# Optimization experiments

Hardware: AMD Instinct MI355X
Metric: run time of the kernel (lower is better)

The kernel has to match this reference:

```python
import jax, jax.numpy as jnp
import numpy as np

LOG_GAIN = 2.5
CLIP_LIMIT = 1.0
GRID = (8, 8)
NBINS = 256
KS = 5
SIGMA_COLOR = 0.1
SIGMA_SPACE = 1.0
SIGMA_G = 1.0


def _gauss1d(ks, sigma):
    x = jnp.arange(ks, dtype=jnp.float32) - ks // 2
    g = jnp.exp(-(x * x) / (2.0 * sigma * sigma))
    return g / g.sum()


def normalize01(x):
    mn, mx = x.min(), x.max()
    return (x - mn) / (mx - mn)


def adjust_log(x, gain):
    # kornia.enhance.adjust_log with clip_output=True
    return jnp.clip(gain * jnp.log2(1.0 + x), 0.0, 1.0)


def equalize_clahe(x, clip_limit, grid, nbins):
    B, C, H, W = x.shape
    GH, GW = grid
    th, tw = H // GH, W // GW
    pixels = th * tw
    # per-tile histograms via flat scatter-add (T = B*C*GH*GW tiles)
    tiles = x.reshape(B, C, GH, th, GW, tw).transpose(0, 1, 2, 4, 3, 5).reshape(-1, pixels)
    bins_t = jnp.clip((tiles * nbins).astype(jnp.int32), 0, nbins - 1)
    T = bins_t.shape[0]
    flat = (jnp.arange(T, dtype=jnp.int32)[:, None] * nbins + bins_t).ravel()
    hist = jnp.zeros((T * nbins,), jnp.float32).at[flat].add(1.0).reshape(T, nbins)
    # clip histogram and redistribute excess uniformly (kornia/OpenCV style)
    max_val = max(int(clip_limit * pixels // nbins), 1)
    clipped = jnp.minimum(hist, float(max_val))
    residual = (pixels - clipped.sum(-1, keepdims=True)) / nbins
    hist = clipped + residual
    lut = jnp.floor(jnp.clip(jnp.cumsum(hist, -1) * ((nbins - 1) / pixels), 0, nbins - 1))
    lut_flat = lut.reshape(B, C, GH * GW * nbins)
    # per-pixel bilinear interpolation between the 4 surrounding tile LUTs
    bin_img = jnp.clip((x * nbins).astype(jnp.int32), 0, nbins - 1)  # (B,C,H,W)
    py = (jnp.arange(H, dtype=jnp.float32) + 0.5) / th - 0.5
    px = (jnp.arange(W, dtype=jnp.float32) + 0.5) / tw - 0.5
    iy0 = jnp.floor(py).astype(jnp.int32); fy = py - iy0
    ix0 = jnp.floor(px).astype(jnp.int32); fx = px - ix0
    iy0c, iy1c = jnp.clip(iy0, 0, GH - 1), jnp.clip(iy0 + 1, 0, GH - 1)
    ix0c, ix1c = jnp.clip(ix0, 0, GW - 1), jnp.clip(ix0 + 1, 0, GW - 1)

    def corner(iy, ix):
        idx = (iy[:, None] * GW + ix[None, :])[None, None] * nbins + bin_img
        return jnp.take_along_axis(lut_flat, idx.reshape(B, C, -1), axis=-1).reshape(B, C, H, W)

    v00, v01 = corner(iy0c, ix0c), corner(iy0c, ix1c)
    v10, v11 = corner(iy1c, ix0c), corner(iy1c, ix1c)
    fy = fy[None, None, :, None]
    fx = fx[None, None, None, :]
    out = (1 - fy) * ((1 - fx) * v00 + fx * v01) + fy * ((1 - fx) * v10 + fx * v11)
    return out / (nbins - 1)


def _neighbors(x, ks):
    # reflect-padded k*k shifted views stacked on a trailing axis
    p = ks // 2
    xp = jnp.pad(x, ((0, 0), (0, 0), (p, p), (p, p)), mode="reflect")
    B, C, H, W = x.shape
    return jnp.stack([xp[:, :, dy:dy + H, dx:dx + W]
                      for dy in range(ks) for dx in range(ks)], axis=-1)


def bilateral_blur(x, ks, sigma_color, sigma_space):
    nb = _neighbors(x, ks)                                   # (B,C,H,W,ks*ks)
    g = _gauss1d(ks, sigma_space)
    space_k = (g[:, None] * g[None, :]).reshape(-1)
    diff = nb - x[..., None]
    # kornia default color_distance_type='l1': (sum_c |diff|)^2
    d2 = jnp.square(jnp.abs(diff).sum(1, keepdims=True))
    kern = jnp.exp((-0.5 / (sigma_color * sigma_color)) * d2) * space_k
    return (nb * kern).sum(-1) / kern.sum(-1)


def gaussian_blur(x, ks, sigma):
    nb = _neighbors(x, ks)
    g = _gauss1d(ks, sigma)
    k2 = (g[:, None] * g[None, :]).reshape(-1)
    return (nb * k2).sum(-1)


def _forward(x):
    x = normalize01(x)
    x = adjust_log(x, LOG_GAIN)
    x = equalize_clahe(x, CLIP_LIMIT, GRID, NBINS)
    x = normalize01(x)
    x = bilateral_blur(x, KS, SIGMA_COLOR, SIGMA_SPACE)
    x = gaussian_blur(x, KS, SIGMA_G)
    return normalize01(x)


def setup_inputs() -> dict:
    key = jax.random.key(0)
    x = jax.random.uniform(key, (16, 1, 512, 512), dtype=jnp.float32)
    return {"x": x}


def reference(x):
    return _forward(x)
```

## Files before the change

### kernel.cpp

```cpp
#include <hip/hip_runtime.h>
#include <stdint.h>

#define HH 512
#define WW 512
#define NBATCH 16
#define IMG (HH*WW)
#define NPIX (NBATCH*IMG)

__device__ __forceinline__ unsigned fkey(float f) {
    unsigned u = __float_as_uint(f);
    return (u & 0x80000000u) ? ~u : (u | 0x80000000u);
}
__device__ __forceinline__ float fdec(unsigned k) {
    unsigned u = (k & 0x80000000u) ? (k ^ 0x80000000u) : ~k;
    return __uint_as_float(u);
}
__device__ __forceinline__ int refl(int i) {
    i = abs(i);
    return (i >= 512) ? (1022 - i) : i;
}
__device__ __forceinline__ float bilerp_lds(const float* __restrict__ slut,
                                            int r0 , int bin,
                                            float fy, float fx) {
    float v00 = slut[r0 + bin];
    float v01 = slut[r0 + 256 + bin];
    float v10 = slut[r0 + 768 + bin];
    float v11 = slut[r0 + 1024 + bin];
    return (1.0f - fy) * ((1.0f - fx) * v00 + fx * v01)
         + fy * ((1.0f - fx) * v10 + fx * v11);
}

__global__ void k_init(unsigned* slots) {
    int t = threadIdx.x;
    if (t < 6) slots[t] = (t & 1) ? 0u : 0xFFFFFFFFu;
}

__global__ __launch_bounds__(256) void k_minmax(const float4* __restrict__ x,
                                                unsigned* slots, int n4) {
    float m = 3.4e38f, M = -3.4e38f;
    for (int i = blockIdx.x * blockDim.x + threadIdx.x; i < n4; i += gridDim.x * blockDim.x) {
        float4 v = x[i];
        m = fminf(m, fminf(fminf(v.x, v.y), fminf(v.z, v.w)));
        M = fmaxf(M, fmaxf(fmaxf(v.x, v.y), fmaxf(v.z, v.w)));
    }
    for (int off = 32; off; off >>= 1) {
        m = fminf(m, __shfl_xor(m, off));
        M = fmaxf(M, __shfl_xor(M, off));
    }
    if ((threadIdx.x & 63) == 0) { atomicMin(slots + 0, fkey(m)); atomicMax(slots + 1, fkey(M)); }
}

__global__ __launch_bounds__(256) void k_hist_lut(const float* __restrict__ x,
                                                  const unsigned* __restrict__ slots,
                                                  unsigned char* __restrict__ bins,
                                                  float* __restrict__ luts) {
    __shared__ int hist[256];
    __shared__ float sc[256];
    int t = threadIdx.x;
    hist[t] = 0;
    int tl = blockIdx.x;
    int b = tl >> 6, ti = tl & 63;
    int row0 = (ti >> 3) * 64, col0 = (ti & 7) * 64;
    float mn = fdec(slots[0]), mx = fdec(slots[1]);
    float rng = mx - mn;
    __syncthreads();
    int tx = t & 63, ty = t >> 6;
    const float* xb = x + b * IMG;
    unsigned char* bb = bins + b * IMG;
    int cnt255 = 0;
    for (int r = 0; r < 16; ++r) {
        int row = row0 + ty + r * 4;
        int idx = row * WW + col0 + tx;
        float z = (xb[idx] - mn) / rng;
        float y = 2.5f * log2f(1.0f + z);
        y = fminf(fmaxf(y, 0.0f), 1.0f);
        int bin = (int)(y * 256.0f);
        bin = min(bin, 255);
        bb[idx] = (unsigned char)bin;
        if (bin == 255) cnt255++;
        else atomicAdd(&hist[bin], 1);
    }
    for (int off = 32; off; off >>= 1) cnt255 += __shfl_xor(cnt255, off);
    if ((t & 63) == 0) atomicAdd(&hist[255], cnt255);
    __syncthreads();
    float cv = fminf((float)hist[t], 16.0f);
    sc[t] = cv;
    __syncthreads();
    for (int off = 1; off < 256; off <<= 1) {
        float add = (t >= off) ? sc[t - off] : 0.0f;
        __syncthreads();
        sc[t] += add;
        __syncthreads();
    }
    float total = sc[255];
    float residual = (4096.0f - total) * (1.0f / 256.0f);
    float cum = sc[t] + (float)(t + 1) * residual;
    float lutv = floorf(fminf(fmaxf(cum * (255.0f / 4096.0f), 0.0f), 255.0f));
    luts[tl * 256 + t] = lutv;
}

__global__ __launch_bounds__(256) void k_clahe_minmax(const unsigned char* __restrict__ bins,
                                                      const float* __restrict__ luts,
                                                      unsigned* slotsOut) {
    __shared__ float slut[9 * 256];
    int t = threadIdx.x;
    int bid = blockIdx.x;
    int b = bid >> 6;
    int ti = bid & 63;
    int tgy = ti >> 3, tgx = ti & 7;
    const float* lb = luts + b * (64 * 256);
    for (int j = t; j < 9 * 256; j += 256) {
        int k = j >> 8;
        int cy = min(max(tgy - 1 + k / 3, 0), 7);
        int cx = min(max(tgx - 1 + k % 3, 0), 7);
        slut[j] = lb[(cy * 8 + cx) * 256 + (j & 255)];
    }
    __syncthreads();
    const unsigned char* bimg = bins + b * IMG;
    int lane = t & 63, wy = t >> 6;
    int gCol = tgx * 64 + lane;
    float px = ((float)gCol + 0.5f) * 0.015625f - 0.5f;
    int ix0 = (int)floorf(px);
    float fx = px - (float)ix0;
    int lx0 = ix0 - tgx + 1;
    float m = 3.4e38f, M = -3.4e38f;
    for (int r = 0; r < 16; ++r) {
        int row = wy + r * 4;
        int gRow = tgy * 64 + row;
        float py = ((float)gRow + 0.5f) * 0.015625f - 0.5f;
        int iy0 = (int)floorf(py);
        float fy = py - (float)iy0;
        int ly0 = iy0 - tgy + 1;
        int r0 = (ly0 * 3 + lx0) << 8;
        int bin = (int)bimg[gRow * WW + gCol];
        float v = bilerp_lds(slut, r0, bin, fy, fx);
        m = fminf(m, v); M = fmaxf(M, v);
    }
    for (int off = 32; off; off >>= 1) {
        m = fminf(m, __shfl_xor(m, off));
        M = fmaxf(M, __shfl_xor(M, off));
    }
    if ((t & 63) == 0) { atomicMin(slotsOut + 0, fkey(m)); atomicMax(slotsOut + 1, fkey(M)); }
}

#define TS 64
#define ZS 72
#define BS 68
__global__ __launch_bounds__(256) void k_bilat_gauss(const unsigned char* __restrict__ bins,
                                                     const float* __restrict__ luts,
                                                     const unsigned* __restrict__ slots,
                                                     float* __restrict__ outg,
                                                     unsigned* slotsOut) {
    __shared__ float z[ZS * ZS];
    __shared__ float sb[BS * BS];
    float* slut = sb;
    int t = threadIdx.x;
    int bid = blockIdx.x;
    int b = bid >> 6;
    int ti = bid & 63;
    int tgy = ti >> 3, tgx = ti & 7;
    int ty0 = tgy * TS, tx0 = tgx * TS;
    const float* lb = luts + b * (64 * 256);
    for (int j = t; j < 9 * 256; j += 256) {
        int k = j >> 8;
        int cy = min(max(tgy - 1 + k / 3, 0), 7);
        int cx = min(max(tgx - 1 + k % 3, 0), 7);
        slut[j] = lb[(cy * 8 + cx) * 256 + (j & 255)];
    }
    __syncthreads();
    float mn = fdec(slots[2]), mx = fdec(slots[3]);
    float inv = 1.0f / (mx - mn);
    const unsigned char* bimg = bins + b * IMG;
    float g0 = expf(-2.0f), g1 = expf(-0.5f);
    float gs = 1.0f + 2.0f * g0 + 2.0f * g1;
    float ga[5] = {g0 / gs, g1 / gs, 1.0f / gs, g1 / gs, g0 / gs};
    for (int j = t; j < ZS * ZS; j += 256) {
        int ly = j / ZS, lx = j - ly * ZS;
        int gy = refl(ty0 - 4 + ly);
        int gx = refl(tx0 - 4 + lx);
        float py = ((float)gy + 0.5f) * 0.015625f - 0.5f;
        float px = ((float)gx + 0.5f) * 0.015625f - 0.5f;
        int iy0 = (int)floorf(py);
        int ix0 = (int)floorf(px);
        float fy = py - (float)iy0;
        float fx = px - (float)ix0;
        int r0 = ((iy0 - tgy + 1) * 3 + (ix0 - tgx + 1)) << 8;
        float v = bilerp_lds(slut, r0, (int)bimg[gy * WW + gx], fy, fx);
        z[j] = (v - mn) * inv;
    }
    __syncthreads();
    for (int j = t; j < BS * BS; j += 256) {
        int ly = j / BS, lx = j - ly * BS;
        int gy = refl(ty0 - 2 + ly);
        int gx = refl(tx0 - 2 + lx);
        int zi = gy - ty0 + 4;
        int zj = gx - tx0 + 4;
        float zc = z[zi * ZS + zj];
        float num = 0.0f, den = 0.0f;
#pragma unroll
        for (int dy = 0; dy < 5; ++dy) {
            float rn = 0.0f, rd = 0.0f;
#pragma unroll
            for (int dx = 0; dx < 5; ++dx) {
                float zn = z[(zi - 2 + dy) * ZS + (zj - 2 + dx)];
                float d = zn - zc;
                float w = __expf(-50.0f * d * d) * ga[dx];
                rn += zn * w;
                rd += w;
            }
            num += ga[dy] * rn;
            den += ga[dy] * rd;
        }
        sb[j] = num / den;
    }
    __syncthreads();
    float* ob = outg + b * IMG;
    float m = 3.4e38f, M = -3.4e38f;
    int ox = t & 63, oy0 = t >> 6;
#pragma unroll
    for (int r = 0; r < 16; ++r) {
        int oy = oy0 + r * 4;
        float s = 0.0f;
#pragma unroll
        for (int dy = 0; dy < 5; ++dy) {
            int bi = (oy + dy) * BS + ox;
            float rs = 0.0f;
#pragma unroll
            for (int dx = 0; dx < 5; ++dx)
                rs += sb[bi + dx] * ga[dx];
            s += rs * ga[dy];
        }
        ob[(ty0 + oy) * WW + tx0 + ox] = s;
        m = fminf(m, s); M = fmaxf(M, s);
    }
    for (int off = 32; off; off >>= 1) {
        m = fminf(m, __shfl_xor(m, off));
        M = fmaxf(M, __shfl_xor(M, off));
    }
    if ((t & 63) == 0) { atomicMin(slotsOut + 0, fkey(m)); atomicMax(slotsOut + 1, fkey(M)); }
}

__global__ __launch_bounds__(256) void k_final(float4* __restrict__ o,
                                               const unsigned* __restrict__ slots, int n4) {
    int i = blockIdx.x * blockDim.x + threadIdx.x;
    if (i >= n4) return;
    float mn = fdec(slots[4]), mx = fdec(slots[5]);
    float rng = mx - mn;
    float4 v = o[i];
    v.x = (v.x - mn) / rng;
    v.y = (v.y - mn) / rng;
    v.z = (v.z - mn) / rng;
    v.w = (v.w - mn) / rng;
    o[i] = v;
}

extern "C" void kernel_launch(void* const* d_in, const int* in_sizes, int n_in,
                              void* d_out, int out_size, void* d_ws, size_t ws_size,
                              hipStream_t stream) {
    const float* x = (const float*)d_in[0];
    float* out = (float*)d_out;
    char* ws = (char*)d_ws;
    unsigned* slots = (unsigned*)ws;
    float* luts = (float*)(ws + 1024);
    unsigned char* bins = (unsigned char*)(ws + 1024 + (1 << 20));

    k_init<<<1, 64, 0, stream>>>(slots);
    k_minmax<<<1024, 256, 0, stream>>>((const float4*)x, slots, NPIX / 4);
    k_hist_lut<<<1024, 256, 0, stream>>>(x, slots, bins, luts);
    k_clahe_minmax<<<1024, 256, 0, stream>>>(bins, luts, slots + 2);
    k_bilat_gauss<<<1024, 256, 0, stream>>>(bins, luts, slots, out, slots + 4);
    k_final<<<4096, 256, 0, stream>>>((float4*)out, slots, NPIX / 4);
}
```

Before: 398.9 us.

## Vectorize histogram/minmax loads, register-tile bilateral, separable gaussian blur

The histogram and CLAHE min/max kernels now handle four adjacent pixels per thread, using float4 and uchar4 loads and stores. The bilateral filter's interior now has each thread compute four horizontally adjacent outputs from a 5x8 register window loaded once from LDS, so neighbour reads are reused. The reflected halo border is handled in a separate loop. The Gaussian blur is split into horizontal and vertical passes, with the intermediate held in the reused z buffer. This cuts LDS traffic and FLOPs, at the cost of more registers and an extra barrier.

```diff
diff --git a/kernel.cpp b/kernel.cpp
--- a/kernel.cpp
+++ b/kernel.cpp
@@ -64,21 +64,32 @@
     float mn = fdec(slots[0]), mx = fdec(slots[1]);
     float rng = mx - mn;
     __syncthreads();
-    int tx = t & 63, ty = t >> 6;
+    int lane = t & 63, wy = t >> 6;
+    int sub = lane & 15, rq = lane >> 4;
+    int cbase = col0 + sub * 4;
     const float* xb = x + b * IMG;
     unsigned char* bb = bins + b * IMG;
     int cnt255 = 0;
-    for (int r = 0; r < 16; ++r) {
-        int row = row0 + ty + r * 4;
-        int idx = row * WW + col0 + tx;
-        float z = (xb[idx] - mn) / rng;
-        float y = 2.5f * log2f(1.0f + z);
-        y = fminf(fmaxf(y, 0.0f), 1.0f);
-        int bin = (int)(y * 256.0f);
-        bin = min(bin, 255);
-        bb[idx] = (unsigned char)bin;
-        if (bin == 255) cnt255++;
-        else atomicAdd(&hist[bin], 1);
+    for (int it = 0; it < 4; ++it) {
+        int row = row0 + it * 16 + wy * 4 + rq;
+        int idx = row * WW + cbase;
+        float4 v4 = *(const float4*)(xb + idx);
+        float vv[4] = {v4.x, v4.y, v4.z, v4.w};
+        uchar4 b4;
+        unsigned char bo[4];
+#pragma unroll
+        for (int k = 0; k < 4; ++k) {
+            float z = (vv[k] - mn) / rng;
+            float y = 2.5f * log2f(1.0f + z);
+            y = fminf(fmaxf(y, 0.0f), 1.0f);
+            int bin = (int)(y * 256.0f);
+            bin = min(bin, 255);
+            bo[k] = (unsigned char)bin;
+            if (bin == 255) cnt255++;
+            else atomicAdd(&hist[bin], 1);
+        }
+        b4.x = bo[0]; b4.y = bo[1]; b4.z = bo[2]; b4.w = bo[3];
+        *(uchar4*)(bb + idx) = b4;
     }
     for (int off = 32; off; off >>= 1) cnt255 += __shfl_xor(cnt255, off);
     if ((t & 63) == 0) atomicAdd(&hist[255], cnt255);
@@ -118,23 +129,33 @@
     __syncthreads();
     const unsigned char* bimg = bins + b * IMG;
     int lane = t & 63, wy = t >> 6;
-    int gCol = tgx * 64 + lane;
-    float px = ((float)gCol + 0.5f) * 0.015625f - 0.5f;
-    int ix0 = (int)floorf(px);
-    float fx = px - (float)ix0;
-    int lx0 = ix0 - tgx + 1;
+    int sub = lane & 15, rq = lane >> 4;
+    int cb = sub * 4;
+    float fxk[4]; int lx0k[4];
+#pragma unroll
+    for (int k = 0; k < 4; ++k) {
+        int gCol = tgx * 64 + cb + k;
+        float px = ((float)gCol + 0.5f) * 0.015625f - 0.5f;
+        int ix0 = (int)floorf(px);
+        fxk[k] = px - (float)ix0;
+        lx0k[k] = ix0 - tgx + 1;
+    }
     float m = 3.4e38f, M = -3.4e38f;
-    for (int r = 0; r < 16; ++r) {
-        int row = wy + r * 4;
+    for (int it = 0; it < 4; ++it) {
+        int row = it * 16 + wy * 4 + rq;
         int gRow = tgy * 64 + row;
         float py = ((float)gRow + 0.5f) * 0.015625f - 0.5f;
         int iy0 = (int)floorf(py);
         float fy = py - (float)iy0;
         int ly0 = iy0 - tgy + 1;
-        int r0 = (ly0 * 3 + lx0) << 8;
-        int bin = (int)bimg[gRow * WW + gCol];
-        float v = bilerp_lds(slut, r0, bin, fy, fx);
-        m = fminf(m, v); M = fmaxf(M, v);
+        uchar4 b4 = *(const uchar4*)(bimg + gRow * WW + tgx * 64 + cb);
+        int ba[4] = {b4.x, b4.y, b4.z, b4.w};
+#pragma unroll
+        for (int k = 0; k < 4; ++k) {
+            int r0 = (ly0 * 3 + lx0k[k]) << 8;
+            float v = bilerp_lds(slut, r0, ba[k], fy, fxk[k]);
+            m = fminf(m, v); M = fmaxf(M, v);
+        }
     }
     for (int off = 32; off; off >>= 1) {
         m = fminf(m, __shfl_xor(m, off));
@@ -189,10 +210,46 @@
         z[j] = (v - mn) * inv;
     }
     __syncthreads();
-    for (int j = t; j < BS * BS; j += 256) {
-        int ly = j / BS, lx = j - ly * BS;
-        int gy = refl(ty0 - 2 + ly);
-        int gx = refl(tx0 - 2 + lx);
+    for (int it = 0; it < 4; ++it) {
+        int task = t + it * 256;
+        int row_t = task >> 4;
+        int col0 = 2 + ((task & 15) << 2);
+        float w[5][8];
+#pragma unroll
+        for (int dy = 0; dy < 5; ++dy)
+#pragma unroll
+            for (int k = 0; k < 8; ++k)
+                w[dy][k] = z[(row_t + 2 + dy) * ZS + (col0 + k)];
+        int sbase = (2 + row_t) * BS + col0;
+#pragma unroll
+        for (int i = 0; i < 4; ++i) {
+            float zc = w[2][i + 2];
+            float num = 0.0f, den = 0.0f;
+#pragma unroll
+            for (int dy = 0; dy < 5; ++dy) {
+                float rn = 0.0f, rd = 0.0f;
+#pragma unroll
+                for (int dx = 0; dx < 5; ++dx) {
+                    float zn = w[dy][i + dx];
+                    float d = zn - zc;
+                    float wt = __expf(-50.0f * d * d) * ga[dx];
+                    rn += zn * wt;
+                    rd += wt;
+                }
+                num += ga[dy] * rn;
+                den += ga[dy] * rd;
+            }
+            sb[sbase + i] = num / den;
+        }
+    }
+    for (int j = t; j < 528; j += 256) {
+        int row, col;
+        if (j < 136)      { row = j / 68;               col = j % 68; }
+        else if (j < 272) { int jj = j - 136; row = 66 + jj / 68; col = jj % 68; }
+        else              { int s = j - 272; row = 2 + (s >> 2);
+                            int c2 = s & 3; col = (c2 & 1) + ((c2 & 2) ? 66 : 0); }
+        int gy = refl(ty0 - 2 + row);
+        int gx = refl(tx0 - 2 + col);
         int zi = gy - ty0 + 4;
         int zj = gx - tx0 + 4;
         float zc = z[zi * ZS + zj];
@@ -204,14 +261,24 @@
             for (int dx = 0; dx < 5; ++dx) {
                 float zn = z[(zi - 2 + dy) * ZS + (zj - 2 + dx)];
                 float d = zn - zc;
-                float w = __expf(-50.0f * d * d) * ga[dx];
-                rn += zn * w;
-                rd += w;
+                float wt = __expf(-50.0f * d * d) * ga[dx];
+                rn += zn * wt;
+                rd += wt;
             }
             num += ga[dy] * rn;
             den += ga[dy] * rd;
         }
-        sb[j] = num / den;
+        sb[row * BS + col] = num / den;
+    }
+    __syncthreads();
+    float* hb = z;
+    for (int j = t; j < 68 * 64; j += 256) {
+        int r = j >> 6, c = j & 63;
+        const float* srow = &sb[r * BS + c];
+        float s = 0.0f;
+#pragma unroll
+        for (int dx = 0; dx < 5; ++dx) s += srow[dx] * ga[dx];
+        hb[j] = s;
     }
     __syncthreads();
     float* ob = outg + b * IMG;
@@ -222,14 +289,8 @@
         int oy = oy0 + r * 4;
         float s = 0.0f;
 #pragma unroll
-        for (int dy = 0; dy < 5; ++dy) {
-            int bi = (oy + dy) * BS + ox;
-            float rs = 0.0f;
-#pragma unroll
-            for (int dx = 0; dx < 5; ++dx)
-                rs += sb[bi + dx] * ga[dx];
-            s += rs * ga[dy];
-        }
+        for (int dy = 0; dy < 5; ++dy)
+            s += hb[(oy + dy) * 64 + ox] * ga[dy];
         ob[(ty0 + oy) * WW + tx0 + ox] = s;
         m = fminf(m, s); M = fmaxf(M, s);
     }
```

Result: faster. 386.8 us (-3.0%).
